# Kernel optimization log

Hardware: AMD Instinct MI355X
Metric: run time of the kernel (lower is better)

The kernel has to match this reference:

```python
import jax, jax.numpy as jnp
import numpy as np

S, L, D = 128, 512, 256   # MSA rows, residues, msa_dim
H, C = 8, 32              # num_heads, head_dim


def setup_inputs() -> dict:
    key = jax.random.key(0)
    ks = jax.random.split(key, 8)
    inp = {
        "msa_input": jax.random.normal(ks[0], (S, L, D), dtype=jnp.float32),
        "ln_scale": jnp.ones((D,), jnp.float32),
        "ln_bias": jnp.zeros((D,), jnp.float32),
        "wq": jax.random.normal(ks[1], (D, H * C), jnp.float32) / np.sqrt(D),
        "wk": jax.random.normal(ks[2], (D, H * C), jnp.float32) / np.sqrt(D),
        "wv": jax.random.normal(ks[3], (D, H * C), jnp.float32) / np.sqrt(D),
        "wg": jax.random.normal(ks[4], (D, H * C), jnp.float32) / np.sqrt(D),
        "bg": jnp.zeros((H * C,), jnp.float32),
        "wo": jax.random.normal(ks[5], (H * C, D), jnp.float32) / np.sqrt(H * C),
        "bo": jnp.zeros((D,), jnp.float32),
    }
    return inp


def reference(msa_input, ln_scale, ln_bias, wq, wk, wv, wg, bg, wo, bo):
    # LayerNorm over last dim (eps matches torch default 1e-5)
    mu = jnp.mean(msa_input, axis=-1, keepdims=True)
    var = jnp.mean(jnp.square(msa_input - mu), axis=-1, keepdims=True)
    x = (msa_input - mu) * jax.lax.rsqrt(var + 1e-5) * ln_scale + ln_bias

    q = (x @ wq).reshape(S, L, H, C)
    k = (x @ wk).reshape(S, L, H, C)
    v = (x @ wv).reshape(S, L, H, C)
    g = jax.nn.sigmoid(x @ wg + bg).reshape(S, L, H, C)

    scale = 1.0 / np.sqrt(C)
    # attention over MSA-row axis, per residue l and head h
    scores = jnp.einsum("slhc,tlhc->stlh", q, k) * scale   # [S,S,L,H]
    probs = jax.nn.softmax(scores, axis=1)                  # softmax over t
    o = jnp.einsum("stlh,tlhc->slhc", probs, v) * g         # [S,L,H,C]
    return o.reshape(S, L, H * C) @ wo + bo
```

## Files before the change

kernel.cpp:

```cpp
#include <hip/hip_runtime.h>
#include <hip/hip_bf16.h>

typedef __bf16 bf16;
typedef __bf16 bf16x8 __attribute__((ext_vector_type(8)));
typedef float f32x4 __attribute__((ext_vector_type(4)));

#define S_DIM 128
#define L_DIM 512
#define D_DIM 256
#define NQ    1024

__device__ __forceinline__ void gl16(void* lds, const void* g) {
  __builtin_amdgcn_global_load_lds((const __attribute__((address_space(1))) void*)g,
                                   (__attribute__((address_space(3))) void*)lds,
                                   16, 0, 0);
}

__global__ void pack_weights(const float* __restrict__ wq, const float* __restrict__ wk,
                             const float* __restrict__ wv, const float* __restrict__ wg,
                             const float* __restrict__ wo,
                             bf16* __restrict__ wcat_t, bf16* __restrict__ wo_t) {
  int idx = blockIdx.x * 256 + threadIdx.x;
  const int total1 = NQ * D_DIM;
  if (idx < total1) {
    int j = idx >> 8;
    int d = idx & 255;
    const float* w = (j < 256) ? wq : (j < 512) ? wk : (j < 768) ? wv : wg;
    wcat_t[idx] = (bf16)w[d * 256 + (j & 255)];
  } else {
    int i2 = idx - total1;
    if (i2 < D_DIM * D_DIM) {
      int dcol = i2 >> 8, k = i2 & 255;
      wo_t[i2] = (bf16)wo[k * 256 + dcol];
    }
  }
}

__global__ __launch_bounds__(256) void ln_kernel(const float* __restrict__ x,
                                                 const float* __restrict__ sc,
                                                 const float* __restrict__ bs,
                                                 bf16* __restrict__ y) {
  const int wid  = threadIdx.x >> 6;
  const int lane = threadIdx.x & 63;
  const int res  = blockIdx.x;
  const int s0   = blockIdx.y * 32;
  float4 scv = ((const float4*)sc)[lane];
  float4 bsv = ((const float4*)bs)[lane];
  #pragma unroll
  for (int it = 0; it < 8; ++it) {
    int s = s0 + it * 4 + wid;
    float4 v = ((const float4*)(x + ((size_t)s * 512 + res) * 256))[lane];
    float sum = v.x + v.y + v.z + v.w;
    #pragma unroll
    for (int m = 32; m; m >>= 1) sum += __shfl_xor(sum, m);
    float mu = sum * (1.0f / 256.0f);
    float dx = v.x - mu, dy = v.y - mu, dz = v.z - mu, dw = v.w - mu;
    float s2 = dx * dx + dy * dy + dz * dz + dw * dw;
    #pragma unroll
    for (int m = 32; m; m >>= 1) s2 += __shfl_xor(s2, m);
    float rs = rsqrtf(s2 * (1.0f / 256.0f) + 1e-5f);
    union { uint2 u; bf16 b[4]; } o;
    o.b[0] = (bf16)(dx * rs * scv.x + bsv.x);
    o.b[1] = (bf16)(dy * rs * scv.y + bsv.y);
    o.b[2] = (bf16)(dz * rs * scv.z + bsv.z);
    o.b[3] = (bf16)(dw * rs * scv.w + bsv.w);
    ((uint2*)y)[((size_t)res * 128 + s) * 64 + lane] = o.u;
  }
}

__device__ __forceinline__ bf16x8 lds_swz(const char* base, int row, int k) {
  return *(const bf16x8*)(base + (((row << 7) + (k << 1)) ^ ((row & 7) << 4)));
}

__global__ __launch_bounds__(512, 4) void gemm_qkvg(const bf16* __restrict__ A,
                                                    const bf16* __restrict__ Bt,
                                                    bf16* __restrict__ pan,
                                                    const float* __restrict__ bias) {
  __shared__ __align__(16) char smem[40960];
  char* As = smem;
  char* Bs = smem + 32768;
  const int tid  = threadIdx.x;
  const int wid  = tid >> 6;
  const int lane = tid & 63;
  const int lrow = lane & 15;
  const int lkg  = lane >> 4;
  const int lk   = lkg * 8;
  const int rb   = lkg * 4;
  const int bid  = blockIdx.x;
  const int n_idx = (bid >> 3) & 15;
  const int m_idx = (bid & 7) | ((bid >> 7) << 3);
  const int m0 = m_idx * 256;
  const int n0 = n_idx * 64;
  const int rg = wid >> 1;
  const int cg = wid & 1;

  const int srow8 = tid >> 3;
  const int slot  = tid & 7;

  f32x4 acc[4][2] = {};

  #pragma unroll
  for (int ks = 0; ks < 4; ++ks) {
    const int k0 = ks * 64;
    #pragma unroll
    for (int p = 0; p < 4; ++p) {
      int r = p * 64 + srow8;
      gl16(As + p * 8192 + wid * 1024,
           A + (size_t)(m0 + r) * 256 + k0 + ((slot ^ (r & 7)) * 8));
    }
    gl16(Bs + wid * 1024,
         Bt + (size_t)(n0 + srow8) * 256 + k0 + ((slot ^ (srow8 & 7)) * 8));
    __syncthreads();
    #pragma unroll
    for (int kk = 0; kk < 64; kk += 32) {
      bf16x8 av[4], bv[2];
      #pragma unroll
      for (int i = 0; i < 4; ++i)
        av[i] = lds_swz(As, rg * 64 + i * 16 + lrow, kk + lk);
      #pragma unroll
      for (int nt = 0; nt < 2; ++nt)
        bv[nt] = lds_swz(Bs, cg * 32 + nt * 16 + lrow, kk + lk);
      #pragma unroll
      for (int i = 0; i < 4; ++i)
        #pragma unroll
        for (int nt = 0; nt < 2; ++nt)
          acc[i][nt] = __builtin_amdgcn_mfma_f32_16x16x32_bf16(av[i], bv[nt], acc[i][nt], 0, 0, 0);
    }
    if (ks < 3) __syncthreads();
  }

  {
    const int type = n_idx >> 2;
    const int hp   = n_idx & 3;
    const bool isg = (type == 3);
    float bgv[2];
    if (isg) {
      bgv[0] = bias[(n_idx - 12) * 64 + cg * 32 + lrow];
      bgv[1] = bias[(n_idx - 12) * 64 + cg * 32 + 16 + lrow];
    }
    const int res = m_idx * 2 + (rg >> 1);
    bf16* pstore = pan + ((size_t)((type * 512 + res) * 4) + hp) * 8192
                 + ((rg & 1) * 64 + rb) * 64 + cg * 32 + lrow;
    #pragma unroll
    for (int i = 0; i < 4; ++i)
      #pragma unroll
      for (int nt = 0; nt < 2; ++nt)
        #pragma unroll
        for (int r = 0; r < 4; ++r) {
          float v = acc[i][nt][r];
          if (isg) { v += bgv[nt]; v = 1.0f / (1.0f + __expf(-v)); }
          pstore[i * 1024 + r * 64 + nt * 16] = (bf16)v;
        }
  }
}

__global__ __launch_bounds__(256, 4) void attn_kernel(const bf16* __restrict__ pan,
                                                      bf16* __restrict__ obuf) {
  __shared__ __align__(16) char smem[40960];
  const int tid  = threadIdx.x;
  const int wid  = tid >> 6;
  const int lane = tid & 63;
  const int lrow = lane & 15;
  const int lkg  = lane >> 4;
  const int lk   = lkg * 8;
  const int rb   = lkg * 4;
  const int bid  = blockIdx.x;
  const int rest = bid >> 3;
  const int hg   = rest & 1;
  const int res  = (bid & 7) | ((rest >> 1) << 3);
  const int h    = hg * 4 + wid;
  const int hp   = h >> 1;
  const int hl   = (h & 1) * 32;

  char* vw  = smem + wid * 8192;
  char* pwb = smem + 32768 + wid * 2048;

  const bf16* Pq = pan + ((size_t)((0 * 512 + res) * 4) + hp) * 8192 + hl;
  const bf16* Pk = pan + ((size_t)((1 * 512 + res) * 4) + hp) * 8192 + hl;
  const bf16* Pv = pan + ((size_t)((2 * 512 + res) * 4) + hp) * 8192 + hl;
  const bf16* Pg = pan + ((size_t)((3 * 512 + res) * 4) + hp) * 8192 + hl;

  {
    int t0 = lane >> 2, cs = (lane & 3) * 8;
    #pragma unroll
    for (int p = 0; p < 8; ++p) {
      int t = p * 16 + t0;
      union { uint4 u; bf16 e[8]; } v;
      v.u = *(const uint4*)(Pv + t * 64 + cs);
      #pragma unroll
      for (int j = 0; j < 8; ++j) {
        int c = cs + j;
        *(bf16*)(vw + ((c * 256 + t * 2) ^ ((c & 7) << 4))) = v.e[j];
      }
    }
  }

  bf16x8 kf[8];
  #pragma unroll
  for (int tt = 0; tt < 8; ++tt)
    kf[tt] = *(const bf16x8*)(Pk + (tt * 16 + lrow) * 64 + lk);

  const float scale = 0.17677669529663687f;
  const f32x4 z = {0.f, 0.f, 0.f, 0.f};

  for (int st = 0; st < 8; ++st) {
    bf16x8 qf = *(const bf16x8*)(Pq + (st * 16 + lrow) * 64 + lk);
    f32x4 sc[8];
    #pragma unroll
    for (int tt = 0; tt < 8; ++tt)
      sc[tt] = __builtin_amdgcn_mfma_f32_16x16x32_bf16(qf, kf[tt], z, 0, 0, 0);

    #pragma unroll
    for (int r = 0; r < 4; ++r) {
      float m = sc[0][r];
      #pragma unroll
      for (int tc = 1; tc < 8; ++tc) m = fmaxf(m, sc[tc][r]);
      #pragma unroll
      for (int msk = 8; msk; msk >>= 1) m = fmaxf(m, __shfl_xor(m, msk));
      float pv[8], ssum = 0.f;
      #pragma unroll
      for (int tc = 0; tc < 8; ++tc) {
        float p = __expf((sc[tc][r] - m) * scale);
        pv[tc] = p; ssum += p;
      }
      #pragma unroll
      for (int msk = 8; msk; msk >>= 1) ssum += __shfl_xor(ssum, msk);
      float inv = 1.0f / ssum;
      #pragma unroll
      for (int tc = 0; tc < 8; ++tc) sc[tc][r] = pv[tc] * inv;
    }

    f32x4 oc[2] = {z, z};
    #pragma unroll
    for (int hf = 0; hf < 2; ++hf) {
      #pragma unroll
      for (int tc = 0; tc < 4; ++tc)
        #pragma unroll
        for (int r = 0; r < 4; ++r) {
          int row = rb + r, col = tc * 16 + lrow;
          *(bf16*)(pwb + ((row * 128 + col * 2) ^ ((row & 7) << 4))) = (bf16)sc[hf * 4 + tc][r];
        }
      #pragma unroll
      for (int kc = 0; kc < 2; ++kc) {
        bf16x8 pa = *(const bf16x8*)(pwb + ((lrow * 128 + (kc * 32 + lk) * 2) ^ ((lrow & 7) << 4)));
        #pragma unroll
        for (int ct = 0; ct < 2; ++ct) {
          int c = ct * 16 + lrow;
          bf16x8 bv = *(const bf16x8*)(vw + ((c * 256 + (hf * 64 + kc * 32 + lk) * 2) ^ ((c & 7) << 4)));
          oc[ct] = __builtin_amdgcn_mfma_f32_16x16x32_bf16(pa, bv, oc[ct], 0, 0, 0);
        }
      }
    }

    #pragma unroll
    for (int ct = 0; ct < 2; ++ct)
      #pragma unroll
      for (int r = 0; r < 4; ++r) {
        int row = rb + r, c = ct * 16 + lrow;
        *(bf16*)(pwb + ((row * 128 + c * 2) ^ ((row & 7) << 4))) = (bf16)oc[ct][r];
      }
    {
      int row = lane >> 2, cb = lane & 3;
      union { uint4 u; bf16 e[8]; } o8, g8, r8;
      o8.u = *(const uint4*)(pwb + ((row * 128 + cb * 16) ^ ((row & 7) << 4)));
      g8.u = *(const uint4*)(Pg + (st * 16 + row) * 64 + cb * 8);
      #pragma unroll
      for (int u = 0; u < 8; ++u) r8.e[u] = (bf16)((float)o8.e[u] * (float)g8.e[u]);
      *(uint4*)(obuf + ((size_t)res * 128 + st * 16 + row) * 256 + h * 32 + cb * 8) = r8.u;
    }
  }
}

__global__ __launch_bounds__(256, 4) void gemm_proj(const bf16* __restrict__ A,
                                                    const bf16* __restrict__ Bt,
                                                    float* __restrict__ Cout,
                                                    const float* __restrict__ bias) {
  __shared__ __align__(16) bf16 smem[16384];
  char* As = (char*)smem;
  char* Bs = (char*)(smem + 8192);
  const int tid  = threadIdx.x;
  const int wid  = tid >> 6;
  const int lane = tid & 63;
  const int bid   = blockIdx.x;
  const int n_idx = (bid >> 3) & 1;
  const int m_idx = (bid & 7) | ((bid >> 4) << 3);
  const int m0 = m_idx * 128;
  const int n0 = n_idx * 128;
  const int lrow = lane & 15;
  const int lk   = (lane >> 4) * 8;
  const int wr = wid >> 1, wc = wid & 1;

  const int ln8 = lane >> 3;
  const int c8  = ((lane & 7) ^ ln8) * 8;

  const bf16* Arow = A  + (size_t)m0 * 256 + c8;
  const bf16* Brow = Bt + (size_t)n0 * 256 + c8;

  f32x4 acc[4][4] = {};

  #pragma unroll
  for (int ks = 0; ks < 4; ++ks) {
    const int k0 = ks * 64;
    #pragma unroll
    for (int t = 0; t < 4; ++t) {
      int chunk = wid * 4 + t;
      int r = chunk * 8 + ln8;
      gl16(As + chunk * 1024, Arow + (size_t)r * 256 + k0);
      gl16(Bs + chunk * 1024, Brow + (size_t)r * 256 + k0);
    }
    __syncthreads();
    #pragma unroll
    for (int kk = 0; kk < 64; kk += 32) {
      bf16x8 av[4], bv[4];
      #pragma unroll
      for (int i = 0; i < 4; ++i)
        av[i] = lds_swz(As, wr * 64 + i * 16 + lrow, kk + lk);
      #pragma unroll
      for (int j = 0; j < 4; ++j)
        bv[j] = lds_swz(Bs, wc * 64 + j * 16 + lrow, kk + lk);
      #pragma unroll
      for (int i = 0; i < 4; ++i)
        #pragma unroll
        for (int j = 0; j < 4; ++j)
          acc[i][j] = __builtin_amdgcn_mfma_f32_16x16x32_bf16(av[i], bv[j], acc[i][j], 0, 0, 0);
    }
    __syncthreads();
  }

  const int rb = (lane >> 4) * 4;
  const int xorv = rb << 2;
  float* smf = (float*)smem;
  float bov[4];
  #pragma unroll
  for (int j = 0; j < 4; ++j) bov[j] = bias[n0 + wc * 64 + j * 16 + lrow];
  #pragma unroll
  for (int half = 0; half < 2; ++half) {
    if (half) __syncthreads();
    #pragma unroll
    for (int i2 = 0; i2 < 2; ++i2) {
      int i = half * 2 + i2;
      #pragma unroll
      for (int j = 0; j < 4; ++j) {
        int col = wc * 64 + j * 16 + lrow;
        #pragma unroll
        for (int r = 0; r < 4; ++r) {
          int crow = wr * 32 + i2 * 16 + rb + r;
          smf[crow * 128 + (col ^ xorv)] = acc[i][j][r] + bov[j];
        }
      }
    }
    __syncthreads();
    #pragma unroll
    for (int p = 0; p < 8; ++p) {
      int ch = p * 256 + tid;
      int crow = ch >> 5, slot = (ch & 31) * 4;
      int rx = (crow & 12) << 2;
      int s_loc = (crow >> 5) * 64 + half * 32 + (crow & 31);
      *(uint4*)(Cout + ((size_t)s_loc * 512 + m_idx) * 256 + n0 + slot) =
          *(const uint4*)(smf + crow * 128 + (slot ^ rx));
    }
  }
}

extern "C" void kernel_launch(void* const* d_in, const int* in_sizes, int n_in,
                              void* d_out, int out_size, void* d_ws, size_t ws_size,
                              hipStream_t stream) {
  const float* msa      = (const float*)d_in[0];
  const float* ln_scale = (const float*)d_in[1];
  const float* ln_bias  = (const float*)d_in[2];
  const float* wq       = (const float*)d_in[3];
  const float* wk       = (const float*)d_in[4];
  const float* wv       = (const float*)d_in[5];
  const float* wg       = (const float*)d_in[6];
  const float* bg       = (const float*)d_in[7];
  const float* wo       = (const float*)d_in[8];
  const float* bo       = (const float*)d_in[9];
  float* out = (float*)d_out;

  char* ws = (char*)d_ws;
  bf16* wcat_t = (bf16*)ws;
  bf16* wo_t   = (bf16*)(ws + 524288);
  bf16* pan    = (bf16*)(ws + 655360);
  bf16* obuf   = (bf16*)(ws + 655360 + 134217728ULL);
  bf16* x_ln2  = (bf16*)d_out;

  pack_weights<<<dim3(1280), dim3(256), 0, stream>>>(wq, wk, wv, wg, wo, wcat_t, wo_t);
  ln_kernel<<<dim3(512, 4), dim3(256), 0, stream>>>(msa, ln_scale, ln_bias, x_ln2);
  gemm_qkvg<<<dim3(4096), dim3(512), 0, stream>>>(x_ln2, wcat_t, pan, bg);
  attn_kernel<<<dim3(1024), dim3(256), 0, stream>>>(pan, obuf);
  gemm_proj<<<dim3(1024), dim3(256), 0, stream>>>(obuf, wo_t, out, bo);
}
```

Before: 149.5 us.

## Fuse QKVG projection into attention kernel, one block per residue

Merges the QKVG GEMM and the row-attention kernel into one kernel. Each 512-thread block loads one residue's 128x256 LayerNormed activations into LDS, and each wave computes its head's K, V, G and Q projections on the fly before doing the attention. This removes the large intermediate QKVG buffer and its round trip through global memory, plus one launch. In exchange it uses about 152 KB of LDS per block and a grid of only 512 blocks, which cuts occupancy and gives less latency hiding. Each wave also reloads its weight slices from global memory.

```diff
diff --git a/kernel.cpp b/kernel.cpp
--- a/kernel.cpp
+++ b/kernel.cpp
@@ -68,17 +68,11 @@
   }
 }
 
-__device__ __forceinline__ bf16x8 lds_swz(const char* base, int row, int k) {
-  return *(const bf16x8*)(base + (((row << 7) + (k << 1)) ^ ((row & 7) << 4)));
-}
-
-__global__ __launch_bounds__(512, 4) void gemm_qkvg(const bf16* __restrict__ A,
-                                                    const bf16* __restrict__ Bt,
-                                                    bf16* __restrict__ pan,
-                                                    const float* __restrict__ bias) {
-  __shared__ __align__(16) char smem[40960];
-  char* As = smem;
-  char* Bs = smem + 32768;
+__global__ __launch_bounds__(512, 2) void qkvg_attn(const bf16* __restrict__ xln,
+                                                    const bf16* __restrict__ wcat,
+                                                    const float* __restrict__ bg,
+                                                    bf16* __restrict__ obuf) {
+  __shared__ __align__(16) char smem[155648];
   const int tid  = threadIdx.x;
   const int wid  = tid >> 6;
   const int lane = tid & 63;
@@ -86,189 +80,202 @@
   const int lkg  = lane >> 4;
   const int lk   = lkg * 8;
   const int rb   = lkg * 4;
-  const int bid  = blockIdx.x;
-  const int n_idx = (bid >> 3) & 15;
-  const int m_idx = (bid & 7) | ((bid >> 7) << 3);
-  const int m0 = m_idx * 256;
-  const int n0 = n_idx * 64;
-  const int rg = wid >> 1;
-  const int cg = wid & 1;
-
-  const int srow8 = tid >> 3;
-  const int slot  = tid & 7;
-
-  f32x4 acc[4][2] = {};
-
-  #pragma unroll
-  for (int ks = 0; ks < 4; ++ks) {
-    const int k0 = ks * 64;
-    #pragma unroll
-    for (int p = 0; p < 4; ++p) {
-      int r = p * 64 + srow8;
-      gl16(As + p * 8192 + wid * 1024,
-           A + (size_t)(m0 + r) * 256 + k0 + ((slot ^ (r & 7)) * 8));
-    }
-    gl16(Bs + wid * 1024,
-         Bt + (size_t)(n0 + srow8) * 256 + k0 + ((slot ^ (srow8 & 7)) * 8));
-    __syncthreads();
-    #pragma unroll
-    for (int kk = 0; kk < 64; kk += 32) {
-      bf16x8 av[4], bv[2];
-      #pragma unroll
-      for (int i = 0; i < 4; ++i)
-        av[i] = lds_swz(As, rg * 64 + i * 16 + lrow, kk + lk);
-      #pragma unroll
-      for (int nt = 0; nt < 2; ++nt)
-        bv[nt] = lds_swz(Bs, cg * 32 + nt * 16 + lrow, kk + lk);
-      #pragma unroll
-      for (int i = 0; i < 4; ++i)
-        #pragma unroll
-        for (int nt = 0; nt < 2; ++nt)
-          acc[i][nt] = __builtin_amdgcn_mfma_f32_16x16x32_bf16(av[i], bv[nt], acc[i][nt], 0, 0, 0);
-    }
-    if (ks < 3) __syncthreads();
-  }
-
-  {
-    const int type = n_idx >> 2;
-    const int hp   = n_idx & 3;
-    const bool isg = (type == 3);
-    float bgv[2];
-    if (isg) {
-      bgv[0] = bias[(n_idx - 12) * 64 + cg * 32 + lrow];
-      bgv[1] = bias[(n_idx - 12) * 64 + cg * 32 + 16 + lrow];
-    }
-    const int res = m_idx * 2 + (rg >> 1);
-    bf16* pstore = pan + ((size_t)((type * 512 + res) * 4) + hp) * 8192
-                 + ((rg & 1) * 64 + rb) * 64 + cg * 32 + lrow;
-    #pragma unroll
-    for (int i = 0; i < 4; ++i)
-      #pragma unroll
-      for (int nt = 0; nt < 2; ++nt)
+  const int res  = blockIdx.x;
+  const int h    = wid;
+
+  char* xlds = smem;
+  char* vw   = smem + 65536 + wid * 8192;
+  char* pwb  = smem + 131072 + wid * 2048;
+  char* scr  = smem + 147456 + wid * 1024;
+
+  {
+    const char* xsrc = (const char*)(xln + (size_t)res * 128 * 256);
+    #pragma unroll
+    for (int p = 0; p < 8; ++p) {
+      int chunk = p * 512 + tid;
+      int row = chunk >> 5, slot = chunk & 31;
+      gl16(xlds + (p * 512 + wid * 64) * 16, xsrc + row * 512 + ((slot ^ (row & 7)) * 16));
+    }
+  }
+  __syncthreads();
+
+  #define LDA(st, kk) (*(const bf16x8*)(xlds + \
+      ((((st) * 16 + lrow) * 512 + ((kk) * 32 + lk) * 2) ^ ((((st) * 16 + lrow) & 7) << 4))))
+
+  const f32x4 z = {0.f, 0.f, 0.f, 0.f};
+  bf16x8 kf[8];
+  bf16  garr[8][2][4];
+
+  {
+    bf16x8 bw[2][8];
+    #pragma unroll
+    for (int cg = 0; cg < 2; ++cg)
+      #pragma unroll
+      for (int kk = 0; kk < 8; ++kk)
+        bw[cg][kk] = *(const bf16x8*)(wcat + (size_t)(256 + h * 32 + cg * 16 + lrow) * 256 + kk * 32 + lk);
+    #pragma unroll
+    for (int st = 0; st < 8; ++st) {
+      f32x4 c0 = z, c1 = z;
+      #pragma unroll
+      for (int kk = 0; kk < 8; ++kk) {
+        bf16x8 a = LDA(st, kk);
+        c0 = __builtin_amdgcn_mfma_f32_16x16x32_bf16(a, bw[0][kk], c0, 0, 0, 0);
+        c1 = __builtin_amdgcn_mfma_f32_16x16x32_bf16(a, bw[1][kk], c1, 0, 0, 0);
+      }
+      #pragma unroll
+      for (int r = 0; r < 4; ++r) {
+        int t = rb + r;
+        *(bf16*)(scr + (((t) * 64 + (lrow) * 2) ^ (((t >> 2) & 3) << 4))) = (bf16)c0[r];
+        *(bf16*)(scr + (((t) * 64 + (16 + lrow) * 2) ^ (((t >> 2) & 3) << 4))) = (bf16)c1[r];
+      }
+      kf[st] = *(const bf16x8*)(scr + ((lrow * 64 + lkg * 16) ^ (((lrow >> 2) & 3) << 4)));
+    }
+  }
+
+  {
+    bf16x8 bw[2][8];
+    #pragma unroll
+    for (int cg = 0; cg < 2; ++cg)
+      #pragma unroll
+      for (int kk = 0; kk < 8; ++kk)
+        bw[cg][kk] = *(const bf16x8*)(wcat + (size_t)(512 + h * 32 + cg * 16 + lrow) * 256 + kk * 32 + lk);
+    #pragma unroll
+    for (int st = 0; st < 8; ++st) {
+      f32x4 c0 = z, c1 = z;
+      #pragma unroll
+      for (int kk = 0; kk < 8; ++kk) {
+        bf16x8 a = LDA(st, kk);
+        c0 = __builtin_amdgcn_mfma_f32_16x16x32_bf16(a, bw[0][kk], c0, 0, 0, 0);
+        c1 = __builtin_amdgcn_mfma_f32_16x16x32_bf16(a, bw[1][kk], c1, 0, 0, 0);
+      }
+      #pragma unroll
+      for (int r = 0; r < 4; ++r) {
+        int t = st * 16 + rb + r;
+        int cA = lrow, cB = 16 + lrow;
+        *(bf16*)(vw + ((cA * 256 + t * 2) ^ ((cA & 7) << 4))) = (bf16)c0[r];
+        *(bf16*)(vw + ((cB * 256 + t * 2) ^ ((cB & 7) << 4))) = (bf16)c1[r];
+      }
+    }
+  }
+
+  {
+    bf16x8 bw[2][8];
+    #pragma unroll
+    for (int cg = 0; cg < 2; ++cg)
+      #pragma unroll
+      for (int kk = 0; kk < 8; ++kk)
+        bw[cg][kk] = *(const bf16x8*)(wcat + (size_t)(768 + h * 32 + cg * 16 + lrow) * 256 + kk * 32 + lk);
+    float bg0 = bg[h * 32 + lrow];
+    float bg1 = bg[h * 32 + 16 + lrow];
+    #pragma unroll
+    for (int st = 0; st < 8; ++st) {
+      f32x4 c0 = z, c1 = z;
+      #pragma unroll
+      for (int kk = 0; kk < 8; ++kk) {
+        bf16x8 a = LDA(st, kk);
+        c0 = __builtin_amdgcn_mfma_f32_16x16x32_bf16(a, bw[0][kk], c0, 0, 0, 0);
+        c1 = __builtin_amdgcn_mfma_f32_16x16x32_bf16(a, bw[1][kk], c1, 0, 0, 0);
+      }
+      #pragma unroll
+      for (int r = 0; r < 4; ++r) {
+        garr[st][0][r] = (bf16)(1.0f / (1.0f + __expf(-(c0[r] + bg0))));
+        garr[st][1][r] = (bf16)(1.0f / (1.0f + __expf(-(c1[r] + bg1))));
+      }
+    }
+  }
+
+  {
+    bf16x8 bw[2][8];
+    #pragma unroll
+    for (int cg = 0; cg < 2; ++cg)
+      #pragma unroll
+      for (int kk = 0; kk < 8; ++kk)
+        bw[cg][kk] = *(const bf16x8*)(wcat + (size_t)(h * 32 + cg * 16 + lrow) * 256 + kk * 32 + lk);
+    const float scale = 0.17677669529663687f;
+
+    for (int st = 0; st < 8; ++st) {
+      f32x4 c0 = z, c1 = z;
+      #pragma unroll
+      for (int kk = 0; kk < 8; ++kk) {
+        bf16x8 a = LDA(st, kk);
+        c0 = __builtin_amdgcn_mfma_f32_16x16x32_bf16(a, bw[0][kk], c0, 0, 0, 0);
+        c1 = __builtin_amdgcn_mfma_f32_16x16x32_bf16(a, bw[1][kk], c1, 0, 0, 0);
+      }
+      #pragma unroll
+      for (int r = 0; r < 4; ++r) {
+        int t = rb + r;
+        *(bf16*)(scr + (((t) * 64 + (lrow) * 2) ^ (((t >> 2) & 3) << 4))) = (bf16)c0[r];
+        *(bf16*)(scr + (((t) * 64 + (16 + lrow) * 2) ^ (((t >> 2) & 3) << 4))) = (bf16)c1[r];
+      }
+      bf16x8 qf = *(const bf16x8*)(scr + ((lrow * 64 + lkg * 16) ^ (((lrow >> 2) & 3) << 4)));
+
+      f32x4 sc[8];
+      #pragma unroll
+      for (int tt = 0; tt < 8; ++tt)
+        sc[tt] = __builtin_amdgcn_mfma_f32_16x16x32_bf16(qf, kf[tt], z, 0, 0, 0);
+
+      #pragma unroll
+      for (int r = 0; r < 4; ++r) {
+        float m = sc[0][r];
+        #pragma unroll
+        for (int tc = 1; tc < 8; ++tc) m = fmaxf(m, sc[tc][r]);
+        #pragma unroll
+        for (int msk = 8; msk; msk >>= 1) m = fmaxf(m, __shfl_xor(m, msk));
+        float pv[8], ssum = 0.f;
+        #pragma unroll
+        for (int tc = 0; tc < 8; ++tc) {
+          float p = __expf((sc[tc][r] - m) * scale);
+          pv[tc] = p; ssum += p;
+        }
+        #pragma unroll
+        for (int msk = 8; msk; msk >>= 1) ssum += __shfl_xor(ssum, msk);
+        float inv = 1.0f / ssum;
+        #pragma unroll
+        for (int tc = 0; tc < 8; ++tc) sc[tc][r] = pv[tc] * inv;
+      }
+
+      f32x4 oc[2] = {z, z};
+      #pragma unroll
+      for (int hf = 0; hf < 2; ++hf) {
+        #pragma unroll
+        for (int tc = 0; tc < 4; ++tc)
+          #pragma unroll
+          for (int r = 0; r < 4; ++r) {
+            int row = rb + r, col = tc * 16 + lrow;
+            *(bf16*)(pwb + ((row * 128 + col * 2) ^ ((row & 7) << 4))) = (bf16)sc[hf * 4 + tc][r];
+          }
+        #pragma unroll
+        for (int kc = 0; kc < 2; ++kc) {
+          bf16x8 pa = *(const bf16x8*)(pwb + ((lrow * 128 + (kc * 32 + lk) * 2) ^ ((lrow & 7) << 4)));
+          #pragma unroll
+          for (int ct = 0; ct < 2; ++ct) {
+            int c = ct * 16 + lrow;
+            bf16x8 bv = *(const bf16x8*)(vw + ((c * 256 + (hf * 64 + kc * 32 + lk) * 2) ^ ((c & 7) << 4)));
+            oc[ct] = __builtin_amdgcn_mfma_f32_16x16x32_bf16(pa, bv, oc[ct], 0, 0, 0);
+          }
+        }
+      }
+
+      #pragma unroll
+      for (int ct = 0; ct < 2; ++ct)
         #pragma unroll
         for (int r = 0; r < 4; ++r) {
-          float v = acc[i][nt][r];
-          if (isg) { v += bgv[nt]; v = 1.0f / (1.0f + __expf(-v)); }
-          pstore[i * 1024 + r * 64 + nt * 16] = (bf16)v;
+          int row = rb + r, c = ct * 16 + lrow;
+          float val = oc[ct][r] * (float)garr[st][ct][r];
+          *(bf16*)(pwb + ((row * 128 + c * 2) ^ ((row & 7) << 4))) = (bf16)val;
         }
-  }
-}
-
-__global__ __launch_bounds__(256, 4) void attn_kernel(const bf16* __restrict__ pan,
-                                                      bf16* __restrict__ obuf) {
-  __shared__ __align__(16) char smem[40960];
-  const int tid  = threadIdx.x;
-  const int wid  = tid >> 6;
-  const int lane = tid & 63;
-  const int lrow = lane & 15;
-  const int lkg  = lane >> 4;
-  const int lk   = lkg * 8;
-  const int rb   = lkg * 4;
-  const int bid  = blockIdx.x;
-  const int rest = bid >> 3;
-  const int hg   = rest & 1;
-  const int res  = (bid & 7) | ((rest >> 1) << 3);
-  const int h    = hg * 4 + wid;
-  const int hp   = h >> 1;
-  const int hl   = (h & 1) * 32;
-
-  char* vw  = smem + wid * 8192;
-  char* pwb = smem + 32768 + wid * 2048;
-
-  const bf16* Pq = pan + ((size_t)((0 * 512 + res) * 4) + hp) * 8192 + hl;
-  const bf16* Pk = pan + ((size_t)((1 * 512 + res) * 4) + hp) * 8192 + hl;
-  const bf16* Pv = pan + ((size_t)((2 * 512 + res) * 4) + hp) * 8192 + hl;
-  const bf16* Pg = pan + ((size_t)((3 * 512 + res) * 4) + hp) * 8192 + hl;
-
-  {
-    int t0 = lane >> 2, cs = (lane & 3) * 8;
-    #pragma unroll
-    for (int p = 0; p < 8; ++p) {
-      int t = p * 16 + t0;
-      union { uint4 u; bf16 e[8]; } v;
-      v.u = *(const uint4*)(Pv + t * 64 + cs);
-      #pragma unroll
-      for (int j = 0; j < 8; ++j) {
-        int c = cs + j;
-        *(bf16*)(vw + ((c * 256 + t * 2) ^ ((c & 7) << 4))) = v.e[j];
-      }
-    }
-  }
-
-  bf16x8 kf[8];
-  #pragma unroll
-  for (int tt = 0; tt < 8; ++tt)
-    kf[tt] = *(const bf16x8*)(Pk + (tt * 16 + lrow) * 64 + lk);
-
-  const float scale = 0.17677669529663687f;
-  const f32x4 z = {0.f, 0.f, 0.f, 0.f};
-
-  for (int st = 0; st < 8; ++st) {
-    bf16x8 qf = *(const bf16x8*)(Pq + (st * 16 + lrow) * 64 + lk);
-    f32x4 sc[8];
-    #pragma unroll
-    for (int tt = 0; tt < 8; ++tt)
-      sc[tt] = __builtin_amdgcn_mfma_f32_16x16x32_bf16(qf, kf[tt], z, 0, 0, 0);
-
-    #pragma unroll
-    for (int r = 0; r < 4; ++r) {
-      float m = sc[0][r];
-      #pragma unroll
-      for (int tc = 1; tc < 8; ++tc) m = fmaxf(m, sc[tc][r]);
-      #pragma unroll
-      for (int msk = 8; msk; msk >>= 1) m = fmaxf(m, __shfl_xor(m, msk));
-      float pv[8], ssum = 0.f;
-      #pragma unroll
-      for (int tc = 0; tc < 8; ++tc) {
-        float p = __expf((sc[tc][r] - m) * scale);
-        pv[tc] = p; ssum += p;
-      }
-      #pragma unroll
-      for (int msk = 8; msk; msk >>= 1) ssum += __shfl_xor(ssum, msk);
-      float inv = 1.0f / ssum;
-      #pragma unroll
-      for (int tc = 0; tc < 8; ++tc) sc[tc][r] = pv[tc] * inv;
-    }
-
-    f32x4 oc[2] = {z, z};
-    #pragma unroll
-    for (int hf = 0; hf < 2; ++hf) {
-      #pragma unroll
-      for (int tc = 0; tc < 4; ++tc)
-        #pragma unroll
-        for (int r = 0; r < 4; ++r) {
-          int row = rb + r, col = tc * 16 + lrow;
-          *(bf16*)(pwb + ((row * 128 + col * 2) ^ ((row & 7) << 4))) = (bf16)sc[hf * 4 + tc][r];
-        }
-      #pragma unroll
-      for (int kc = 0; kc < 2; ++kc) {
-        bf16x8 pa = *(const bf16x8*)(pwb + ((lrow * 128 + (kc * 32 + lk) * 2) ^ ((lrow & 7) << 4)));
-        #pragma unroll
-        for (int ct = 0; ct < 2; ++ct) {
-          int c = ct * 16 + lrow;
-          bf16x8 bv = *(const bf16x8*)(vw + ((c * 256 + (hf * 64 + kc * 32 + lk) * 2) ^ ((c & 7) << 4)));
-          oc[ct] = __builtin_amdgcn_mfma_f32_16x16x32_bf16(pa, bv, oc[ct], 0, 0, 0);
-        }
-      }
-    }
-
-    #pragma unroll
-    for (int ct = 0; ct < 2; ++ct)
-      #pragma unroll
-      for (int r = 0; r < 4; ++r) {
-        int row = rb + r, c = ct * 16 + lrow;
-        *(bf16*)(pwb + ((row * 128 + c * 2) ^ ((row & 7) << 4))) = (bf16)oc[ct][r];
-      }
-    {
-      int row = lane >> 2, cb = lane & 3;
-      union { uint4 u; bf16 e[8]; } o8, g8, r8;
-      o8.u = *(const uint4*)(pwb + ((row * 128 + cb * 16) ^ ((row & 7) << 4)));
-      g8.u = *(const uint4*)(Pg + (st * 16 + row) * 64 + cb * 8);
-      #pragma unroll
-      for (int u = 0; u < 8; ++u) r8.e[u] = (bf16)((float)o8.e[u] * (float)g8.e[u]);
-      *(uint4*)(obuf + ((size_t)res * 128 + st * 16 + row) * 256 + h * 32 + cb * 8) = r8.u;
-    }
-  }
+      {
+        int row = lane >> 2, cb = lane & 3;
+        uint4 o8 = *(const uint4*)(pwb + ((row * 128 + cb * 16) ^ ((row & 7) << 4)));
+        *(uint4*)(obuf + ((size_t)res * 128 + st * 16 + row) * 256 + h * 32 + cb * 8) = o8;
+      }
+    }
+  }
+  #undef LDA
+}
+
+__device__ __forceinline__ bf16x8 lds_swz(const char* base, int row, int k) {
+  return *(const bf16x8*)(base + (((row << 7) + (k << 1)) ^ ((row & 7) << 4)));
 }
 
 __global__ __launch_bounds__(256, 4) void gemm_proj(const bf16* __restrict__ A,
@@ -380,13 +387,11 @@
   char* ws = (char*)d_ws;
   bf16* wcat_t = (bf16*)ws;
   bf16* wo_t   = (bf16*)(ws + 524288);
-  bf16* pan    = (bf16*)(ws + 655360);
-  bf16* obuf   = (bf16*)(ws + 655360 + 134217728ULL);
-  bf16* x_ln2  = (bf16*)d_out;
+  bf16* obuf   = (bf16*)(ws + 655360);
+  bf16* x_ln2  = (bf16*)(ws + 655360 + 33554432ULL);
 
   pack_weights<<<dim3(1280), dim3(256), 0, stream>>>(wq, wk, wv, wg, wo, wcat_t, wo_t);
   ln_kernel<<<dim3(512, 4), dim3(256), 0, stream>>>(msa, ln_scale, ln_bias, x_ln2);
-  gemm_qkvg<<<dim3(4096), dim3(512), 0, stream>>>(x_ln2, wcat_t, pan, bg);
-  attn_kernel<<<dim3(1024), dim3(256), 0, stream>>>(pan, obuf);
+  qkvg_attn<<<dim3(512), dim3(512), 0, stream>>>(x_ln2, wcat_t, bg, obuf);
   gemm_proj<<<dim3(1024), dim3(256), 0, stream>>>(obuf, wo_t, out, bo);
 }
```

Measured after the change: 201.6 us. 1.35x slower.
